# Optimization experiments

Hardware: AMD Instinct MI355X
Metric: run time of the kernel (lower is better)

Reference implementation:

```python
import jax, jax.numpy as jnp
import numpy as np

N, D = 8192, 256
TEMP = 0.07


def setup_inputs() -> dict:
    key = jax.random.key(0)
    kx, ky = jax.random.split(key)
    x = jax.random.normal(kx, (N, D), dtype=jnp.float32)
    y = jax.random.normal(ky, (N, D), dtype=jnp.float32)
    # L2-normalize (standard for InfoNCE; keeps exp(sim/temp) finite)
    x = x / jnp.linalg.norm(x, axis=-1, keepdims=True)
    y = y / jnp.linalg.norm(y, axis=-1, keepdims=True)
    return {"x": x, "y": y}


def reference(x, y):
    # sim_matrix = exp(x @ y^T / temperature), shape [N, N]
    sim = jnp.exp(jnp.matmul(x, y.T) / TEMP)
    # positives: exp(<x_i, y_i>/T) == diagonal of sim
    l_pos = jnp.exp(jnp.sum(x * y, axis=-1) / TEMP)
    # negatives: row-sum excluding the diagonal (equivalent to masked_select)
    l_neg = jnp.sum(sim, axis=-1) - jnp.diagonal(sim)
    loss = jnp.mean(-jnp.log(l_pos / l_neg))
    return loss
```

## Files before the change

### kernel.cpp

```cpp
#include <hip/hip_runtime.h>
#include <hip/hip_bf16.h>

#define N_ROWS 8192
#define D_DIM  256

static constexpr float kQuantScale = 64.0f;
static constexpr float kScaleAcc = 20.609929155556627f / 4096.0f;
static constexpr float kInvTAcc  = 14.285714285714286f / 4096.0f;

typedef float f32x4 __attribute__((ext_vector_type(4)));
typedef int   i32x4 __attribute__((ext_vector_type(4)));
typedef int   i32x8 __attribute__((ext_vector_type(8)));

__device__ __forceinline__ void gl_lds16(const void* g, void* l) {
  __builtin_amdgcn_global_load_lds(
      (const __attribute__((address_space(1))) void*)g,
      (__attribute__((address_space(3))) void*)l, 16, 0, 0);
}

__global__ __launch_bounds__(256)
void cvt_fp8_kernel(const float* __restrict__ x, const float* __restrict__ y,
                    unsigned char* __restrict__ xq, unsigned char* __restrict__ yq,
                    float* __restrict__ rowsum, unsigned int* __restrict__ done) {
  if (blockIdx.x == 0) {
    for (int i = threadIdx.x; i < N_ROWS; i += 256) rowsum[i] = 0.f;
    if (threadIdx.x == 0) *done = 0u;
  }
  const int per_mat = N_ROWS * D_DIM / 8;
  int idx = blockIdx.x * blockDim.x + threadIdx.x;
  const float* src = x;
  unsigned char* dst = xq;
  int i = idx;
  if (idx >= per_mat) { src = y; dst = yq; i = idx - per_mat; }
  float4 a = ((const float4*)src)[2 * (size_t)i];
  float4 b = ((const float4*)src)[2 * (size_t)i + 1];
  int v0 = 0, v1 = 0;
  v0 = __builtin_amdgcn_cvt_pk_fp8_f32(a.x * kQuantScale, a.y * kQuantScale, v0, false);
  v0 = __builtin_amdgcn_cvt_pk_fp8_f32(a.z * kQuantScale, a.w * kQuantScale, v0, true);
  v1 = __builtin_amdgcn_cvt_pk_fp8_f32(b.x * kQuantScale, b.y * kQuantScale, v1, false);
  v1 = __builtin_amdgcn_cvt_pk_fp8_f32(b.z * kQuantScale, b.w * kQuantScale, v1, true);
  *(int2*)(dst + (size_t)i * 8) = make_int2(v0, v1);
}

__global__ __launch_bounds__(512, 1)
void infonce_gemm(const unsigned char* __restrict__ X,
                  const unsigned char* __restrict__ Y,
                  float* __restrict__ rowsum, float* __restrict__ diag,
                  unsigned int* __restrict__ done, float* __restrict__ out) {
  __shared__ unsigned char Xs[256 * 256];
  __shared__ unsigned char Ys[2][128 * 256];
  __shared__ unsigned int ticket_s;

  const int b  = blockIdx.x;
  const int bi = b >> 3;
  const int gj = b & 7;

  const int t    = threadIdx.x;
  const int lane = t & 63;
  const int wave = t >> 6;
  const int wm   = wave >> 1;
  const int wn   = wave & 1;
  const int quad = lane >> 4;
  const int l15  = lane & 15;

  const unsigned char* Xblk = X + (size_t)(bi * 256) * D_DIM;

#pragma unroll
  for (int it = 0; it < 8; ++it) {
    const int c0  = (it * 8 + wave) * 64;
    const int s   = c0 + lane;
    const int row = s >> 4;
    const int cg  = (s & 15) ^ (row & 15);
    gl_lds16(Xblk + (size_t)row * D_DIM + cg * 16, &Xs[c0 * 16]);
  }
  {
    const unsigned char* Yblk = Y + (size_t)(gj * 8) * 128 * D_DIM;
#pragma unroll
    for (int it = 0; it < 4; ++it) {
      const int c0  = (it * 8 + wave) * 64;
      const int s   = c0 + lane;
      const int row = s >> 4;
      const int cg  = (s & 15) ^ (row & 15);
      gl_lds16(Yblk + (size_t)row * D_DIM + cg * 16, &Ys[0][c0 * 16]);
    }
  }

  f32x4 acc[4][4];
#pragma unroll
  for (int a = 0; a < 4; ++a)
#pragma unroll
    for (int c = 0; c < 4; ++c) acc[a][c] = (f32x4){0.f, 0.f, 0.f, 0.f};

  float psum[4][4];
#pragma unroll
  for (int a = 0; a < 4; ++a)
#pragma unroll
    for (int c = 0; c < 4; ++c) psum[a][c] = 0.f;

  for (int tt = 0; tt < 8; ++tt) {
    const int p = tt & 1;

    __syncthreads();

    if (tt < 7) {
      const unsigned char* Yblk = Y + (size_t)(gj * 8 + tt + 1) * 128 * D_DIM;
#pragma unroll
      for (int it = 0; it < 4; ++it) {
        const int c0  = (it * 8 + wave) * 64;
        const int s   = c0 + lane;
        const int row = s >> 4;
        const int cg  = (s & 15) ^ (row & 15);
        gl_lds16(Yblk + (size_t)row * D_DIM + cg * 16, &Ys[p ^ 1][c0 * 16]);
      }
    }

#pragma unroll
    for (int kb = 0; kb < 2; ++kb) {
      i32x8 a8[4], b8[4];
#pragma unroll
      for (int mt = 0; mt < 4; ++mt) {
        const int row = wm * 64 + mt * 16 + l15;
        const int p0  = (kb * 8 + quad * 2 + 0) ^ (row & 15);
        const int p1  = (kb * 8 + quad * 2 + 1) ^ (row & 15);
        i32x4 lo = *(const i32x4*)(&Xs[row * 256 + p0 * 16]);
        i32x4 hi = *(const i32x4*)(&Xs[row * 256 + p1 * 16]);
        a8[mt] = __builtin_shufflevector(lo, hi, 0, 1, 2, 3, 4, 5, 6, 7);
      }
#pragma unroll
      for (int nt = 0; nt < 4; ++nt) {
        const int row = wn * 64 + nt * 16 + l15;
        const int p0  = (kb * 8 + quad * 2 + 0) ^ (row & 15);
        const int p1  = (kb * 8 + quad * 2 + 1) ^ (row & 15);
        i32x4 lo = *(const i32x4*)(&Ys[p][row * 256 + p0 * 16]);
        i32x4 hi = *(const i32x4*)(&Ys[p][row * 256 + p1 * 16]);
        b8[nt] = __builtin_shufflevector(lo, hi, 0, 1, 2, 3, 4, 5, 6, 7);
      }
#pragma unroll
      for (int mt = 0; mt < 4; ++mt)
#pragma unroll
        for (int nt = 0; nt < 4; ++nt)
          acc[mt][nt] = __builtin_amdgcn_mfma_scale_f32_16x16x128_f8f6f4(
              a8[mt], b8[nt], acc[mt][nt],
              0, 0,
              0, 0x7F7F7F7F,
              0, 0x7F7F7F7F);
    }

#pragma unroll
    for (int mt = 0; mt < 4; ++mt) {
#pragma unroll
      for (int rr = 0; rr < 4; ++rr) {
        float part = 0.f;
#pragma unroll
        for (int nt = 0; nt < 4; ++nt)
          part += __builtin_amdgcn_exp2f(acc[mt][nt][rr] * kScaleAcc);
        psum[mt][rr] += part;
      }
    }
    {
      const int ct = gj * 8 + tt;
      const bool d0 = (ct == 2 * bi)     && (wm == wn);
      const bool d1 = (ct == 2 * bi + 1) && (wm == wn + 2);
      if (d0 || d1) {
        const int gi_base = bi * 256 + wm * 64;
#pragma unroll
        for (int nt = 0; nt < 4; ++nt)
#pragma unroll
          for (int rr = 0; rr < 4; ++rr)
            if (l15 == quad * 4 + rr)
              atomicExch(&diag[gi_base + nt * 16 + l15], acc[nt][nt][rr]);
      }
    }
#pragma unroll
    for (int a = 0; a < 4; ++a)
#pragma unroll
      for (int c = 0; c < 4; ++c) acc[a][c] = (f32x4){0.f, 0.f, 0.f, 0.f};
  }

  {
    const int gi_base = bi * 256 + wm * 64;
#pragma unroll
    for (int mt = 0; mt < 4; ++mt) {
#pragma unroll
      for (int rr = 0; rr < 4; ++rr) {
        float v = psum[mt][rr];
        v += __shfl_xor(v, 1);
        v += __shfl_xor(v, 2);
        v += __shfl_xor(v, 4);
        v += __shfl_xor(v, 8);
        if (l15 == 0)
          atomicAdd(&rowsum[gi_base + mt * 16 + quad * 4 + rr], v);
      }
    }
  }

  __syncthreads();
  if (t == 0) ticket_s = atomicAdd(done, 1u);
  __syncthreads();
  if (ticket_s == 255u) {
    __threadfence();
    float local = 0.f;
    for (int i = t; i < N_ROWS; i += 512) {
      const float rs = atomicAdd(&rowsum[i], 0.0f);
      const float d  = atomicAdd(&diag[i], 0.0f);
      local += __logf(rs - __builtin_amdgcn_exp2f(d * kScaleAcc)) - d * kInvTAcc;
    }
    float* red = (float*)Xs;
    red[t] = local;
    __syncthreads();
    for (int s2 = 256; s2 > 0; s2 >>= 1) {
      if (t < s2) red[t] += red[t + s2];
      __syncthreads();
    }
    if (t == 0) out[0] = red[0] / (float)N_ROWS;
  }
}

extern "C" void kernel_launch(void* const* d_in, const int* in_sizes, int n_in,
                              void* d_out, int out_size, void* d_ws, size_t ws_size,
                              hipStream_t stream) {
  const float* x = (const float*)d_in[0];
  const float* y = (const float*)d_in[1];
  float* out = (float*)d_out;

  float* rowsum = (float*)d_ws;
  float* diag   = rowsum + N_ROWS;
  unsigned int* done = (unsigned int*)(diag + N_ROWS);
  unsigned char* xq = (unsigned char*)d_ws + 2 * N_ROWS * sizeof(float) + 16;
  unsigned char* yq = xq + (size_t)N_ROWS * D_DIM;

  int cvt_blocks = 2 * N_ROWS * D_DIM / 8 / 256;
  cvt_fp8_kernel<<<cvt_blocks, 256, 0, stream>>>(x, y, xq, yq, rowsum, done);

  infonce_gemm<<<256, 512, 0, stream>>>(xq, yq, rowsum, diag, done, out);
}
```

Measured before the change: 100.9 us.

## Hoist X fragments into registers and distribute final reduction per row-block

The X tile fragments are now loaded from LDS into registers once, before the N-tile loop, rather than being reloaded on every iteration. This removes repeated LDS reads at the cost of more live registers. The global completion ticket is split into per-row-block counters, so the last of the 8 blocks sharing a row block reduces its own 256 rows with wave shuffles and atomically adds the result to the output. This replaces a single last block that serially reduced all 8192 rows, at the cost of a float atomicAdd on the output, which makes the summation order nondeterministic.

```diff
diff --git a/kernel.cpp b/kernel.cpp
--- a/kernel.cpp
+++ b/kernel.cpp
@@ -21,10 +21,12 @@
 __global__ __launch_bounds__(256)
 void cvt_fp8_kernel(const float* __restrict__ x, const float* __restrict__ y,
                     unsigned char* __restrict__ xq, unsigned char* __restrict__ yq,
-                    float* __restrict__ rowsum, unsigned int* __restrict__ done) {
+                    float* __restrict__ rowsum, unsigned int* __restrict__ done,
+                    float* __restrict__ out) {
   if (blockIdx.x == 0) {
     for (int i = threadIdx.x; i < N_ROWS; i += 256) rowsum[i] = 0.f;
-    if (threadIdx.x == 0) *done = 0u;
+    if (threadIdx.x < 32) done[threadIdx.x] = 0u;
+    if (threadIdx.x == 32) out[0] = 0.f;
   }
   const int per_mat = N_ROWS * D_DIM / 8;
   int idx = blockIdx.x * blockDim.x + threadIdx.x;
@@ -85,6 +87,22 @@
     }
   }
 
+  __syncthreads();
+
+  i32x8 a8r[2][4];
+#pragma unroll
+  for (int kb = 0; kb < 2; ++kb) {
+#pragma unroll
+    for (int mt = 0; mt < 4; ++mt) {
+      const int row = wm * 64 + mt * 16 + l15;
+      const int p0  = (kb * 8 + quad * 2 + 0) ^ (row & 15);
+      const int p1  = (kb * 8 + quad * 2 + 1) ^ (row & 15);
+      i32x4 lo = *(const i32x4*)(&Xs[row * 256 + p0 * 16]);
+      i32x4 hi = *(const i32x4*)(&Xs[row * 256 + p1 * 16]);
+      a8r[kb][mt] = __builtin_shufflevector(lo, hi, 0, 1, 2, 3, 4, 5, 6, 7);
+    }
+  }
+
   f32x4 acc[4][4];
 #pragma unroll
   for (int a = 0; a < 4; ++a)
@@ -100,7 +118,7 @@
   for (int tt = 0; tt < 8; ++tt) {
     const int p = tt & 1;
 
-    __syncthreads();
+    if (tt) __syncthreads();
 
     if (tt < 7) {
       const unsigned char* Yblk = Y + (size_t)(gj * 8 + tt + 1) * 128 * D_DIM;
@@ -116,16 +134,7 @@
 
 #pragma unroll
     for (int kb = 0; kb < 2; ++kb) {
-      i32x8 a8[4], b8[4];
-#pragma unroll
-      for (int mt = 0; mt < 4; ++mt) {
-        const int row = wm * 64 + mt * 16 + l15;
-        const int p0  = (kb * 8 + quad * 2 + 0) ^ (row & 15);
-        const int p1  = (kb * 8 + quad * 2 + 1) ^ (row & 15);
-        i32x4 lo = *(const i32x4*)(&Xs[row * 256 + p0 * 16]);
-        i32x4 hi = *(const i32x4*)(&Xs[row * 256 + p1 * 16]);
-        a8[mt] = __builtin_shufflevector(lo, hi, 0, 1, 2, 3, 4, 5, 6, 7);
-      }
+      i32x8 b8[4];
 #pragma unroll
       for (int nt = 0; nt < 4; ++nt) {
         const int row = wn * 64 + nt * 16 + l15;
@@ -140,7 +149,7 @@
 #pragma unroll
         for (int nt = 0; nt < 4; ++nt)
           acc[mt][nt] = __builtin_amdgcn_mfma_scale_f32_16x16x128_f8f6f4(
-              a8[mt], b8[nt], acc[mt][nt],
+              a8r[kb][mt], b8[nt], acc[mt][nt],
               0, 0,
               0, 0x7F7F7F7F,
               0, 0x7F7F7F7F);
@@ -195,24 +204,32 @@
   }
 
   __syncthreads();
-  if (t == 0) ticket_s = atomicAdd(done, 1u);
+  if (t == 0) ticket_s = atomicAdd(&done[bi], 1u);
   __syncthreads();
-  if (ticket_s == 255u) {
+  if (ticket_s == 7u) {
     __threadfence();
     float local = 0.f;
-    for (int i = t; i < N_ROWS; i += 512) {
+    if (t < 256) {
+      const int i = bi * 256 + t;
       const float rs = atomicAdd(&rowsum[i], 0.0f);
       const float d  = atomicAdd(&diag[i], 0.0f);
-      local += __logf(rs - __builtin_amdgcn_exp2f(d * kScaleAcc)) - d * kInvTAcc;
-    }
+      local = __logf(rs - __builtin_amdgcn_exp2f(d * kScaleAcc)) - d * kInvTAcc;
+    }
+    local += __shfl_down(local, 32);
+    local += __shfl_down(local, 16);
+    local += __shfl_down(local, 8);
+    local += __shfl_down(local, 4);
+    local += __shfl_down(local, 2);
+    local += __shfl_down(local, 1);
     float* red = (float*)Xs;
-    red[t] = local;
+    if (lane == 0) red[wave] = local;
     __syncthreads();
-    for (int s2 = 256; s2 > 0; s2 >>= 1) {
-      if (t < s2) red[t] += red[t + s2];
-      __syncthreads();
-    }
-    if (t == 0) out[0] = red[0] / (float)N_ROWS;
+    if (t == 0) {
+      float s = 0.f;
+#pragma unroll
+      for (int w = 0; w < 8; ++w) s += red[w];
+      atomicAdd(out, s / (float)N_ROWS);
+    }
   }
 }
 
@@ -226,11 +243,11 @@
   float* rowsum = (float*)d_ws;
   float* diag   = rowsum + N_ROWS;
   unsigned int* done = (unsigned int*)(diag + N_ROWS);
-  unsigned char* xq = (unsigned char*)d_ws + 2 * N_ROWS * sizeof(float) + 16;
+  unsigned char* xq = (unsigned char*)d_ws + 2 * N_ROWS * sizeof(float) + 128;
   unsigned char* yq = xq + (size_t)N_ROWS * D_DIM;
 
   int cvt_blocks = 2 * N_ROWS * D_DIM / 8 / 256;
-  cvt_fp8_kernel<<<cvt_blocks, 256, 0, stream>>>(x, y, xq, yq, rowsum, done);
+  cvt_fp8_kernel<<<cvt_blocks, 256, 0, stream>>>(x, y, xq, yq, rowsum, done, out);
 
   infonce_gemm<<<256, 512, 0, stream>>>(xq, yq, rowsum, diag, done, out);
 }
```

New measurement: 105.0 us. 1.04x slower.

## Deepen Y-tile pipeline to four 64-row buffers with deferred exp epilogue

Applied to the files above, without the earlier changes.

Splits each Y tile into 64-row chunks held in a 4-deep LDS ring, prefetched three tiles ahead and synchronised with explicit vmcnt waits and raw s_barriers instead of __syncthreads. The exp/rowsum epilogue of the previous tile is deferred so it interleaves with the next tile's MFMA work, and MFMA issue is wrapped in raised wave priority. The intent is to hide global-to-LDS latency and overlap transcendental work with matrix ops. In exchange there are more, smaller iterations with more barriers per tile, and correctness now depends on hand-counted waitcnt values.

```diff
diff --git a/kernel.cpp b/kernel.cpp
--- a/kernel.cpp
+++ b/kernel.cpp
@@ -11,6 +11,8 @@
 typedef float f32x4 __attribute__((ext_vector_type(4)));
 typedef int   i32x4 __attribute__((ext_vector_type(4)));
 typedef int   i32x8 __attribute__((ext_vector_type(8)));
+
+#define WAITV(n) asm volatile("s_waitcnt vmcnt(" #n ")" ::: "memory")
 
 __device__ __forceinline__ void gl_lds16(const void* g, void* l) {
   __builtin_amdgcn_global_load_lds(
@@ -21,10 +23,12 @@
 __global__ __launch_bounds__(256)
 void cvt_fp8_kernel(const float* __restrict__ x, const float* __restrict__ y,
                     unsigned char* __restrict__ xq, unsigned char* __restrict__ yq,
-                    float* __restrict__ rowsum, unsigned int* __restrict__ done) {
+                    float* __restrict__ rowsum, unsigned int* __restrict__ done,
+                    float* __restrict__ out) {
   if (blockIdx.x == 0) {
     for (int i = threadIdx.x; i < N_ROWS; i += 256) rowsum[i] = 0.f;
-    if (threadIdx.x == 0) *done = 0u;
+    if (threadIdx.x < 32) done[threadIdx.x] = 0u;
+    if (threadIdx.x == 32) out[0] = 0.f;
   }
   const int per_mat = N_ROWS * D_DIM / 8;
   int idx = blockIdx.x * blockDim.x + threadIdx.x;
@@ -48,7 +52,7 @@
                   float* __restrict__ rowsum, float* __restrict__ diag,
                   unsigned int* __restrict__ done, float* __restrict__ out) {
   __shared__ unsigned char Xs[256 * 256];
-  __shared__ unsigned char Ys[2][128 * 256];
+  __shared__ unsigned char Ys[4][64 * 256];
   __shared__ unsigned int ticket_s;
 
   const int b  = blockIdx.x;
@@ -65,6 +69,18 @@
 
   const unsigned char* Xblk = X + (size_t)(bi * 256) * D_DIM;
 
+  auto stageY = [&](int tile, int buf) {
+#pragma unroll
+    for (int it = 0; it < 2; ++it) {
+      const int c0  = (it * 8 + wave) * 64;
+      const int s   = c0 + lane;
+      const int row = s >> 4;
+      const int cg  = (s & 15) ^ (row & 15);
+      gl_lds16(Y + (size_t)(gj * 1024 + tile * 64 + row) * D_DIM + cg * 16,
+               &Ys[buf][c0 * 16]);
+    }
+  };
+
 #pragma unroll
   for (int it = 0; it < 8; ++it) {
     const int c0  = (it * 8 + wave) * 64;
@@ -73,23 +89,17 @@
     const int cg  = (s & 15) ^ (row & 15);
     gl_lds16(Xblk + (size_t)row * D_DIM + cg * 16, &Xs[c0 * 16]);
   }
-  {
-    const unsigned char* Yblk = Y + (size_t)(gj * 8) * 128 * D_DIM;
-#pragma unroll
-    for (int it = 0; it < 4; ++it) {
-      const int c0  = (it * 8 + wave) * 64;
-      const int s   = c0 + lane;
-      const int row = s >> 4;
-      const int cg  = (s & 15) ^ (row & 15);
-      gl_lds16(Yblk + (size_t)row * D_DIM + cg * 16, &Ys[0][c0 * 16]);
-    }
-  }
-
-  f32x4 acc[4][4];
+  stageY(0, 0);
+  stageY(1, 1);
+  stageY(2, 2);
+  WAITV(4);
+  __builtin_amdgcn_s_barrier();
+
+  f32x4 acc[4][2];
 #pragma unroll
   for (int a = 0; a < 4; ++a)
 #pragma unroll
-    for (int c = 0; c < 4; ++c) acc[a][c] = (f32x4){0.f, 0.f, 0.f, 0.f};
+    for (int c = 0; c < 2; ++c) acc[a][c] = (f32x4){0.f, 0.f, 0.f, 0.f};
 
   float psum[4][4];
 #pragma unroll
@@ -97,85 +107,86 @@
 #pragma unroll
     for (int c = 0; c < 4; ++c) psum[a][c] = 0.f;
 
-  for (int tt = 0; tt < 8; ++tt) {
-    const int p = tt & 1;
-
-    __syncthreads();
-
-    if (tt < 7) {
-      const unsigned char* Yblk = Y + (size_t)(gj * 8 + tt + 1) * 128 * D_DIM;
-#pragma unroll
-      for (int it = 0; it < 4; ++it) {
-        const int c0  = (it * 8 + wave) * 64;
-        const int s   = c0 + lane;
-        const int row = s >> 4;
-        const int cg  = (s & 15) ^ (row & 15);
-        gl_lds16(Yblk + (size_t)row * D_DIM + cg * 16, &Ys[p ^ 1][c0 * 16]);
-      }
-    }
+  auto do_epilogue = [&](const int rt) {
+#pragma unroll
+    for (int mt = 0; mt < 4; ++mt) {
+#pragma unroll
+      for (int rr = 0; rr < 4; ++rr) {
+        psum[mt][rr] += __builtin_amdgcn_exp2f(acc[mt][0][rr] * kScaleAcc)
+                      + __builtin_amdgcn_exp2f(acc[mt][1][rr] * kScaleAcc);
+      }
+    }
+    const int h = gj * 16 + rt - 4 * bi;
+    if (h >= 0 && h < 4 && wm == h) {
+#pragma unroll
+      for (int nt = 0; nt < 2; ++nt)
+#pragma unroll
+        for (int rr = 0; rr < 4; ++rr)
+          if (l15 == quad * 4 + rr)
+            atomicExch(&diag[bi * 256 + wm * 64 + (wn * 2 + nt) * 16 + l15],
+                       acc[wn * 2 + nt][nt][rr]);
+    }
+#pragma unroll
+    for (int a = 0; a < 4; ++a)
+#pragma unroll
+      for (int c = 0; c < 2; ++c) acc[a][c] = (f32x4){0.f, 0.f, 0.f, 0.f};
+  };
+
+#pragma unroll
+  for (int tt = 0; tt < 16; ++tt) {
+    const int buf = tt & 3;
+
+    if (tt > 0) do_epilogue(tt - 1);
 
 #pragma unroll
     for (int kb = 0; kb < 2; ++kb) {
-      i32x8 a8[4], b8[4];
+      i32x8 a8[4], b8[2];
 #pragma unroll
       for (int mt = 0; mt < 4; ++mt) {
         const int row = wm * 64 + mt * 16 + l15;
-        const int p0  = (kb * 8 + quad * 2 + 0) ^ (row & 15);
-        const int p1  = (kb * 8 + quad * 2 + 1) ^ (row & 15);
+        const int p0  = (kb * 8 + quad * 2) ^ (row & 15);
         i32x4 lo = *(const i32x4*)(&Xs[row * 256 + p0 * 16]);
-        i32x4 hi = *(const i32x4*)(&Xs[row * 256 + p1 * 16]);
+        i32x4 hi = *(const i32x4*)(&Xs[row * 256 + (p0 ^ 1) * 16]);
         a8[mt] = __builtin_shufflevector(lo, hi, 0, 1, 2, 3, 4, 5, 6, 7);
       }
 #pragma unroll
-      for (int nt = 0; nt < 4; ++nt) {
-        const int row = wn * 64 + nt * 16 + l15;
-        const int p0  = (kb * 8 + quad * 2 + 0) ^ (row & 15);
-        const int p1  = (kb * 8 + quad * 2 + 1) ^ (row & 15);
-        i32x4 lo = *(const i32x4*)(&Ys[p][row * 256 + p0 * 16]);
-        i32x4 hi = *(const i32x4*)(&Ys[p][row * 256 + p1 * 16]);
+      for (int nt = 0; nt < 2; ++nt) {
+        const int row = wn * 32 + nt * 16 + l15;
+        const int p0  = (kb * 8 + quad * 2) ^ (row & 15);
+        i32x4 lo = *(const i32x4*)(&Ys[buf][row * 256 + p0 * 16]);
+        i32x4 hi = *(const i32x4*)(&Ys[buf][row * 256 + (p0 ^ 1) * 16]);
         b8[nt] = __builtin_shufflevector(lo, hi, 0, 1, 2, 3, 4, 5, 6, 7);
       }
+
+      if (kb == 0 && tt + 3 < 16) stageY(tt + 3, (tt + 3) & 3);
+
+      __builtin_amdgcn_sched_barrier(0);
+      __builtin_amdgcn_s_barrier();
+
+      __builtin_amdgcn_s_setprio(1);
 #pragma unroll
       for (int mt = 0; mt < 4; ++mt)
 #pragma unroll
-        for (int nt = 0; nt < 4; ++nt)
+        for (int nt = 0; nt < 2; ++nt)
           acc[mt][nt] = __builtin_amdgcn_mfma_scale_f32_16x16x128_f8f6f4(
               a8[mt], b8[nt], acc[mt][nt],
               0, 0,
               0, 0x7F7F7F7F,
               0, 0x7F7F7F7F);
-    }
-
-#pragma unroll
-    for (int mt = 0; mt < 4; ++mt) {
-#pragma unroll
-      for (int rr = 0; rr < 4; ++rr) {
-        float part = 0.f;
-#pragma unroll
-        for (int nt = 0; nt < 4; ++nt)
-          part += __builtin_amdgcn_exp2f(acc[mt][nt][rr] * kScaleAcc);
-        psum[mt][rr] += part;
-      }
-    }
-    {
-      const int ct = gj * 8 + tt;
-      const bool d0 = (ct == 2 * bi)     && (wm == wn);
-      const bool d1 = (ct == 2 * bi + 1) && (wm == wn + 2);
-      if (d0 || d1) {
-        const int gi_base = bi * 256 + wm * 64;
-#pragma unroll
-        for (int nt = 0; nt < 4; ++nt)
-#pragma unroll
-          for (int rr = 0; rr < 4; ++rr)
-            if (l15 == quad * 4 + rr)
-              atomicExch(&diag[gi_base + nt * 16 + l15], acc[nt][nt][rr]);
-      }
-    }
-#pragma unroll
-    for (int a = 0; a < 4; ++a)
-#pragma unroll
-      for (int c = 0; c < 4; ++c) acc[a][c] = (f32x4){0.f, 0.f, 0.f, 0.f};
-  }
+      __builtin_amdgcn_s_setprio(0);
+
+      if (kb == 0) {
+        __builtin_amdgcn_s_barrier();
+      } else {
+        if (tt <= 12)      { WAITV(4); }
+        else if (tt == 13) { WAITV(2); }
+        else if (tt == 14) { WAITV(0); }
+        if (tt < 15) __builtin_amdgcn_s_barrier();
+      }
+    }
+  }
+
+  do_epilogue(15);
 
   {
     const int gi_base = bi * 256 + wm * 64;
@@ -195,7 +206,7 @@
   }
 
   __syncthreads();
-  if (t == 0) ticket_s = atomicAdd(done, 1u);
+  if (t == 0) ticket_s = atomicAdd(&done[0], 1u);
   __syncthreads();
   if (ticket_s == 255u) {
     __threadfence();
@@ -226,11 +237,11 @@
   float* rowsum = (float*)d_ws;
   float* diag   = rowsum + N_ROWS;
   unsigned int* done = (unsigned int*)(diag + N_ROWS);
-  unsigned char* xq = (unsigned char*)d_ws + 2 * N_ROWS * sizeof(float) + 16;
+  unsigned char* xq = (unsigned char*)d_ws + 2 * N_ROWS * sizeof(float) + 128;
   unsigned char* yq = xq + (size_t)N_ROWS * D_DIM;
 
   int cvt_blocks = 2 * N_ROWS * D_DIM / 8 / 256;
-  cvt_fp8_kernel<<<cvt_blocks, 256, 0, stream>>>(x, y, xq, yq, rowsum, done);
+  cvt_fp8_kernel<<<cvt_blocks, 256, 0, stream>>>(x, y, xq, yq, rowsum, done, out);
 
   infonce_gemm<<<256, 512, 0, stream>>>(xq, yq, rowsum, diag, done, out);
 }
```

New measurement: 195.2 us. +93.5%, slower.

## Drop LDS staging; read fp8 tiles directly from global with more, smaller blocks

Applied to the files above, without the earlier changes.

Replaces the LDS-staged, double-buffered 256x128 tiling with a scheme where each of 1024 blocks (256 threads) handles 64 rows and 1024 columns. Each wave loads its MFMA operands straight from global memory and relies on L2/L1 caching instead of shared memory. Row sums are pre-reduced in a small shared array before the global atomics, and the completion ticket threshold is updated for the larger grid. This raises occupancy and removes LDS traffic and barriers, at the cost of redundant global/cache reads of X and Y and no explicit load/compute overlap.

```diff
diff --git a/kernel.cpp b/kernel.cpp
--- a/kernel.cpp
+++ b/kernel.cpp
@@ -12,19 +12,15 @@
 typedef int   i32x4 __attribute__((ext_vector_type(4)));
 typedef int   i32x8 __attribute__((ext_vector_type(8)));
 
-__device__ __forceinline__ void gl_lds16(const void* g, void* l) {
-  __builtin_amdgcn_global_load_lds(
-      (const __attribute__((address_space(1))) void*)g,
-      (__attribute__((address_space(3))) void*)l, 16, 0, 0);
-}
-
 __global__ __launch_bounds__(256)
 void cvt_fp8_kernel(const float* __restrict__ x, const float* __restrict__ y,
                     unsigned char* __restrict__ xq, unsigned char* __restrict__ yq,
-                    float* __restrict__ rowsum, unsigned int* __restrict__ done) {
+                    float* __restrict__ rowsum, unsigned int* __restrict__ done,
+                    float* __restrict__ out) {
   if (blockIdx.x == 0) {
     for (int i = threadIdx.x; i < N_ROWS; i += 256) rowsum[i] = 0.f;
-    if (threadIdx.x == 0) *done = 0u;
+    if (threadIdx.x < 32) done[threadIdx.x] = 0u;
+    if (threadIdx.x == 32) out[0] = 0.f;
   }
   const int per_mat = N_ROWS * D_DIM / 8;
   int idx = blockIdx.x * blockDim.x + threadIdx.x;
@@ -42,54 +38,30 @@
   *(int2*)(dst + (size_t)i * 8) = make_int2(v0, v1);
 }
 
-__global__ __launch_bounds__(512, 1)
+__global__ __launch_bounds__(256)
 void infonce_gemm(const unsigned char* __restrict__ X,
                   const unsigned char* __restrict__ Y,
                   float* __restrict__ rowsum, float* __restrict__ diag,
                   unsigned int* __restrict__ done, float* __restrict__ out) {
-  __shared__ unsigned char Xs[256 * 256];
-  __shared__ unsigned char Ys[2][128 * 256];
+  __shared__ float sm[64];
+  __shared__ float red[256];
   __shared__ unsigned int ticket_s;
 
   const int b  = blockIdx.x;
-  const int bi = b >> 3;
-  const int gj = b & 7;
+  const int bR = b >> 3;
+  const int bC = b & 7;
 
   const int t    = threadIdx.x;
   const int lane = t & 63;
-  const int wave = t >> 6;
-  const int wm   = wave >> 1;
-  const int wn   = wave & 1;
+  const int w    = t >> 6;
   const int quad = lane >> 4;
   const int l15  = lane & 15;
 
-  const unsigned char* Xblk = X + (size_t)(bi * 256) * D_DIM;
+  if (t < 64) sm[t] = 0.f;
+  __syncthreads();
 
-#pragma unroll
-  for (int it = 0; it < 8; ++it) {
-    const int c0  = (it * 8 + wave) * 64;
-    const int s   = c0 + lane;
-    const int row = s >> 4;
-    const int cg  = (s & 15) ^ (row & 15);
-    gl_lds16(Xblk + (size_t)row * D_DIM + cg * 16, &Xs[c0 * 16]);
-  }
-  {
-    const unsigned char* Yblk = Y + (size_t)(gj * 8) * 128 * D_DIM;
-#pragma unroll
-    for (int it = 0; it < 4; ++it) {
-      const int c0  = (it * 8 + wave) * 64;
-      const int s   = c0 + lane;
-      const int row = s >> 4;
-      const int cg  = (s & 15) ^ (row & 15);
-      gl_lds16(Yblk + (size_t)row * D_DIM + cg * 16, &Ys[0][c0 * 16]);
-    }
-  }
-
-  f32x4 acc[4][4];
-#pragma unroll
-  for (int a = 0; a < 4; ++a)
-#pragma unroll
-    for (int c = 0; c < 4; ++c) acc[a][c] = (f32x4){0.f, 0.f, 0.f, 0.f};
+  const int rowbase = bR * 64;
+  const unsigned char* Xr = X + (size_t)rowbase * D_DIM;
 
   float psum[4][4];
 #pragma unroll
@@ -97,42 +69,31 @@
 #pragma unroll
     for (int c = 0; c < 4; ++c) psum[a][c] = 0.f;
 
-  for (int tt = 0; tt < 8; ++tt) {
-    const int p = tt & 1;
+  for (int jt = 0; jt < 4; ++jt) {
+    const int cbase = bC * 1024 + w * 256 + jt * 64;
+    const unsigned char* Yc = Y + (size_t)cbase * D_DIM;
 
-    __syncthreads();
-
-    if (tt < 7) {
-      const unsigned char* Yblk = Y + (size_t)(gj * 8 + tt + 1) * 128 * D_DIM;
+    f32x4 acc[4][4];
 #pragma unroll
-      for (int it = 0; it < 4; ++it) {
-        const int c0  = (it * 8 + wave) * 64;
-        const int s   = c0 + lane;
-        const int row = s >> 4;
-        const int cg  = (s & 15) ^ (row & 15);
-        gl_lds16(Yblk + (size_t)row * D_DIM + cg * 16, &Ys[p ^ 1][c0 * 16]);
-      }
-    }
+    for (int a = 0; a < 4; ++a)
+#pragma unroll
+      for (int c = 0; c < 4; ++c) acc[a][c] = (f32x4){0.f, 0.f, 0.f, 0.f};
 
 #pragma unroll
     for (int kb = 0; kb < 2; ++kb) {
       i32x8 a8[4], b8[4];
 #pragma unroll
       for (int mt = 0; mt < 4; ++mt) {
-        const int row = wm * 64 + mt * 16 + l15;
-        const int p0  = (kb * 8 + quad * 2 + 0) ^ (row & 15);
-        const int p1  = (kb * 8 + quad * 2 + 1) ^ (row & 15);
-        i32x4 lo = *(const i32x4*)(&Xs[row * 256 + p0 * 16]);
-        i32x4 hi = *(const i32x4*)(&Xs[row * 256 + p1 * 16]);
+        const size_t off = (size_t)(mt * 16 + l15) * D_DIM + kb * 128 + quad * 32;
+        i32x4 lo = *(const i32x4*)(Xr + off);
+        i32x4 hi = *(const i32x4*)(Xr + off + 16);
         a8[mt] = __builtin_shufflevector(lo, hi, 0, 1, 2, 3, 4, 5, 6, 7);
       }
 #pragma unroll
       for (int nt = 0; nt < 4; ++nt) {
-        const int row = wn * 64 + nt * 16 + l15;
-        const int p0  = (kb * 8 + quad * 2 + 0) ^ (row & 15);
-        const int p1  = (kb * 8 + quad * 2 + 1) ^ (row & 15);
-        i32x4 lo = *(const i32x4*)(&Ys[p][row * 256 + p0 * 16]);
-        i32x4 hi = *(const i32x4*)(&Ys[p][row * 256 + p1 * 16]);
+        const size_t off = (size_t)(nt * 16 + l15) * D_DIM + kb * 128 + quad * 32;
+        i32x4 lo = *(const i32x4*)(Yc + off);
+        i32x4 hi = *(const i32x4*)(Yc + off + 16);
         b8[nt] = __builtin_shufflevector(lo, hi, 0, 1, 2, 3, 4, 5, 6, 7);
       }
 #pragma unroll
@@ -157,58 +118,46 @@
         psum[mt][rr] += part;
       }
     }
-    {
-      const int ct = gj * 8 + tt;
-      const bool d0 = (ct == 2 * bi)     && (wm == wn);
-      const bool d1 = (ct == 2 * bi + 1) && (wm == wn + 2);
-      if (d0 || d1) {
-        const int gi_base = bi * 256 + wm * 64;
+    if (cbase == rowbase) {
 #pragma unroll
-        for (int nt = 0; nt < 4; ++nt)
+      for (int nt = 0; nt < 4; ++nt)
 #pragma unroll
-          for (int rr = 0; rr < 4; ++rr)
-            if (l15 == quad * 4 + rr)
-              atomicExch(&diag[gi_base + nt * 16 + l15], acc[nt][nt][rr]);
-      }
-    }
-#pragma unroll
-    for (int a = 0; a < 4; ++a)
-#pragma unroll
-      for (int c = 0; c < 4; ++c) acc[a][c] = (f32x4){0.f, 0.f, 0.f, 0.f};
-  }
-
-  {
-    const int gi_base = bi * 256 + wm * 64;
-#pragma unroll
-    for (int mt = 0; mt < 4; ++mt) {
-#pragma unroll
-      for (int rr = 0; rr < 4; ++rr) {
-        float v = psum[mt][rr];
-        v += __shfl_xor(v, 1);
-        v += __shfl_xor(v, 2);
-        v += __shfl_xor(v, 4);
-        v += __shfl_xor(v, 8);
-        if (l15 == 0)
-          atomicAdd(&rowsum[gi_base + mt * 16 + quad * 4 + rr], v);
-      }
+        for (int rr = 0; rr < 4; ++rr)
+          if (l15 == quad * 4 + rr)
+            atomicExch(&diag[rowbase + nt * 16 + l15], acc[nt][nt][rr]);
     }
   }
 
+#pragma unroll
+  for (int mt = 0; mt < 4; ++mt) {
+#pragma unroll
+    for (int rr = 0; rr < 4; ++rr) {
+      float v = psum[mt][rr];
+      v += __shfl_xor(v, 1);
+      v += __shfl_xor(v, 2);
+      v += __shfl_xor(v, 4);
+      v += __shfl_xor(v, 8);
+      if (l15 == 0)
+        atomicAdd(&sm[mt * 16 + quad * 4 + rr], v);
+    }
+  }
   __syncthreads();
-  if (t == 0) ticket_s = atomicAdd(done, 1u);
+  if (t < 64) atomicAdd(&rowsum[rowbase + t], sm[t]);
+
   __syncthreads();
-  if (ticket_s == 255u) {
+  if (t == 0) ticket_s = atomicAdd(&done[0], 1u);
+  __syncthreads();
+  if (ticket_s == 1023u) {
     __threadfence();
     float local = 0.f;
-    for (int i = t; i < N_ROWS; i += 512) {
+    for (int i = t; i < N_ROWS; i += 256) {
       const float rs = atomicAdd(&rowsum[i], 0.0f);
       const float d  = atomicAdd(&diag[i], 0.0f);
       local += __logf(rs - __builtin_amdgcn_exp2f(d * kScaleAcc)) - d * kInvTAcc;
     }
-    float* red = (float*)Xs;
     red[t] = local;
     __syncthreads();
-    for (int s2 = 256; s2 > 0; s2 >>= 1) {
+    for (int s2 = 128; s2 > 0; s2 >>= 1) {
       if (t < s2) red[t] += red[t + s2];
       __syncthreads();
     }
@@ -226,11 +175,11 @@
   float* rowsum = (float*)d_ws;
   float* diag   = rowsum + N_ROWS;
   unsigned int* done = (unsigned int*)(diag + N_ROWS);
-  unsigned char* xq = (unsigned char*)d_ws + 2 * N_ROWS * sizeof(float) + 16;
+  unsigned char* xq = (unsigned char*)d_ws + 2 * N_ROWS * sizeof(float) + 128;
   unsigned char* yq = xq + (size_t)N_ROWS * D_DIM;
 
   int cvt_blocks = 2 * N_ROWS * D_DIM / 8 / 256;
-  cvt_fp8_kernel<<<cvt_blocks, 256, 0, stream>>>(x, y, xq, yq, rowsum, done);
+  cvt_fp8_kernel<<<cvt_blocks, 256, 0, stream>>>(x, y, xq, yq, rowsum, done, out);
 
-  infonce_gemm<<<256, 512, 0, stream>>>(xq, yq, rowsum, diag, done, out);
+  infonce_gemm<<<1024, 256, 0, stream>>>(xq, yq, rowsum, diag, done, out);
 }
```

Measured after the change: 121.3 us. 1.2x slower.
